# Performance work log

Hardware: AMD Instinct MI355X
Metric: run time of the kernel (lower is better)

The kernel has to match this reference:

```python
import jax, jax.numpy as jnp
import numpy as np


def setup_inputs() -> dict:
    key = jax.random.key(0)
    k1, k2, k3 = jax.random.split(key, 3)
    T, B, C, H, W = 8, 4, 128, 96, 96
    h = w = 384  # original visibility-map resolution
    values = jax.random.normal(k1, (T + 1, B, C, H, W), jnp.float32)
    tvmap = jax.random.uniform(k2, (B, 1, h, w), jnp.float32)
    rvmaps = jax.random.uniform(k3, (T, B, 1, h, w), jnp.float32)
    return {"values": values, "tvmap": tvmap, "rvmaps": rvmaps}


def _resize_bin(m, H, W):
    # bilinear resize (half-pixel centers == torch align_corners=False), then > 0.5 threshold
    r = jax.image.resize(m, m.shape[:-2] + (H, W), method="bilinear")
    return (r > 0.5).astype(m.dtype)


def reference(values, tvmap, rvmaps):
    t_feat = values[0]          # [B,C,H,W]
    r_feats = values[1:]        # [T,B,C,H,W]
    T, B, C, H, W = r_feats.shape

    tv = _resize_bin(tvmap, H, W)                           # [B,1,H,W]
    rv = jax.vmap(lambda m: _resize_bin(m, H, W))(rvmaps)   # [T,B,1,H,W]
    vmap_ = tv[None] * rv                                   # [T,B,1,H,W]

    # per-frame masked similarity score gs
    gs = jnp.sum(vmap_ * t_feat[None] * r_feats, axis=(-1, -2, -3))  # [T,B]
    v_sum = jnp.sum(vmap_[:, :, 0], axis=(-1, -2))                   # [T,B]
    empty = v_sum < 1e-4
    gs = jnp.where(empty, 0.0, gs) / (v_sum + empty.astype(gs.dtype)) / C

    gss = gs.transpose(1, 0)[:, None, :, None, None]   # [B,1,T,1,1]
    vmaps = rv.transpose(1, 2, 0, 3, 4)                # [B,1,T,H,W]

    # masked softmax over frame axis (dim=2) with zero-guard
    mv = gss * vmaps
    mx = jnp.max(mv, axis=2, keepdims=True)
    me = jnp.exp(mv - mx) * vmaps
    ms = jnp.sum(me, axis=2, keepdims=True)
    ms = ms + (ms < 1e-4).astype(ms.dtype)
    c_match = jax.lax.stop_gradient(me / ms)           # [B,1,T,H,W]

    rf = r_feats.transpose(1, 2, 0, 3, 4)              # [B,C,T,H,W]
    c_out = jnp.sum(rf * c_match, axis=2)              # [B,C,H,W]

    c_mask = jnp.sum(c_match * vmaps, axis=2)          # [B,1,H,W]
    c_mask = jax.lax.stop_gradient(1.0 - jnp.mean(c_mask, axis=1, keepdims=True))

    out = jnp.concatenate([t_feat, c_out, c_mask], axis=1)  # [B, 2C+1, H, W]
    return out, c_mask, gs
```

## Files before the change

kernel.cpp:

```cpp
#include <hip/hip_runtime.h>
#include <math.h>

#define T_ 8
#define B_ 4
#define C_ 128
#define HW_ 9216
#define IN_HW_ 147456

__device__ __forceinline__ double resize_px(const float* __restrict__ img, int y, int x) {
  static const double wm[8]  = {0.03125, 0.09375, 0.15625, 0.21875,
                                0.21875, 0.15625, 0.09375, 0.03125};
  static const double w0[8]  = {0.0, 0.0, 0.625/3.5, 0.875/3.5,
                                0.875/3.5, 0.625/3.5, 0.375/3.5, 0.125/3.5};
  static const double w95[8] = {0.125/3.5, 0.375/3.5, 0.625/3.5, 0.875/3.5,
                                0.875/3.5, 0.625/3.5, 0.0, 0.0};
  const double* wy = (y == 0) ? w0 : (y == 95 ? w95 : wm);
  const double* wx = (x == 0) ? w0 : (x == 95 ? w95 : wm);
  double acc = 0.0;
#pragma unroll
  for (int ky = 0; ky < 8; ++ky) {
    double wyv = wy[ky];
    if (wyv == 0.0) continue;
    int jy = 4 * y - 2 + ky;
    const float* row = img + jy * 384;
    double ra = 0.0;
#pragma unroll
    for (int kx = 0; kx < 8; ++kx) {
      double wxv = wx[kx];
      if (wxv == 0.0) continue;
      int jx = 4 * x - 2 + kx;
      ra += wxv * (double)row[jx];
    }
    acc += wyv * ra;
  }
  return acc;
}

__device__ __forceinline__ float block_reduce_sum_256(float v) {
  __shared__ float s[256];
  s[threadIdx.x] = v;
  __syncthreads();
  for (int k = 128; k > 0; k >>= 1) {
    if (threadIdx.x < (unsigned)k) s[threadIdx.x] += s[threadIdx.x + k];
    __syncthreads();
  }
  return s[0];
}

__global__ void k_init(float* __restrict__ v_sum) {
  if (threadIdx.x < T_ * B_) v_sum[threadIdx.x] = 0.f;
}

__global__ void k_tv(const float* __restrict__ tvmap, float* __restrict__ tv) {
  int b = blockIdx.y;
  int p = blockIdx.x * 256 + threadIdx.x;
  const float* img = tvmap + (size_t)b * IN_HW_;
  int y = p / 96, x = p % 96;
  tv[(size_t)b * HW_ + p] = (resize_px(img, y, x) > 0.5) ? 1.0f : 0.0f;
}

__global__ void k_rv(const float* __restrict__ rvmaps, const float* __restrict__ tv,
                     float* __restrict__ rv, float* __restrict__ vm,
                     float* __restrict__ v_sum) {
  int tb = blockIdx.y;
  int b = tb % B_;
  int p = blockIdx.x * 256 + threadIdx.x;
  const float* img = rvmaps + (size_t)tb * IN_HW_;
  int y = p / 96, x = p % 96;
  float rvv = (resize_px(img, y, x) > 0.5) ? 1.0f : 0.0f;
  float vmv = rvv * tv[(size_t)b * HW_ + p];
  rv[(size_t)tb * HW_ + p] = rvv;
  vm[(size_t)tb * HW_ + p] = vmv;
  float s = block_reduce_sum_256(vmv);
  if (threadIdx.x == 0) atomicAdd(&v_sum[tb], s);
}

__global__ __launch_bounds__(256) void k_gs(const float* __restrict__ values,
                                            const float* __restrict__ vm,
                                            float* __restrict__ gs_part) {
  int blk = blockIdx.x;
  int c  = blk % C_;
  int tb = blk / C_;
  int b  = tb % B_;
  const float4* rf  = (const float4*)(values + ((size_t)(B_ + tb) * C_ + c) * HW_);
  const float4* tf  = (const float4*)(values + ((size_t)b * C_ + c) * HW_);
  const float4* vmp = (const float4*)(vm + (size_t)tb * HW_);
  float acc = 0.f;
  for (int i = threadIdx.x; i < HW_ / 4; i += 256) {
    float4 m = vmp[i];
    float4 a = tf[i];
    float4 r = rf[i];
    acc += m.x * a.x * r.x + m.y * a.y * r.y + m.z * a.z * r.z + m.w * a.w * r.w;
  }
  float s = block_reduce_sum_256(acc);
  if (threadIdx.x == 0) gs_part[blk] = s;
}

__global__ void k_gsfin(const float* __restrict__ gs_part, const float* __restrict__ v_sum,
                        float* __restrict__ gs, float* __restrict__ out_gs) {
  int i = threadIdx.x;
  if (i < T_ * B_) {
    float s = 0.f;
    for (int c = 0; c < C_; ++c) s += gs_part[i * C_ + c];
    float vs = v_sum[i];
    bool empty = vs < 1e-4f;
    float g = (empty ? 0.f : s) / (vs + (empty ? 1.f : 0.f)) / (float)C_;
    gs[i] = g;
    out_gs[i] = g;
  }
}

__global__ __launch_bounds__(256) void k_epi(const float* __restrict__ values,
                                             const float* __restrict__ rv,
                                             const float* __restrict__ gs,
                                             float* __restrict__ out,
                                             float* __restrict__ out_cmask) {
  int ctile = blockIdx.x;
  int ptile = blockIdx.y;
  int b     = blockIdx.z;
  __shared__ float gsh[T_];
  if (threadIdx.x < T_) gsh[threadIdx.x] = gs[threadIdx.x * B_ + b];
  __syncthreads();

  int p0 = ptile * 1024 + threadIdx.x * 4;

  float4 rv4[T_];
#pragma unroll
  for (int t = 0; t < T_; ++t)
    rv4[t] = *(const float4*)(rv + ((size_t)(t * B_ + b)) * HW_ + p0);

  float cm[T_][4];
  float cmask[4];
#pragma unroll
  for (int j = 0; j < 4; ++j) {
    float mv[T_];
    float mx = -1e30f;
#pragma unroll
    for (int t = 0; t < T_; ++t) {
      float rvv = ((const float*)&rv4[t])[j];
      mv[t] = gsh[t] * rvv;
      mx = fmaxf(mx, mv[t]);
    }
    float e[T_];
    float ms = 0.f;
#pragma unroll
    for (int t = 0; t < T_; ++t) {
      float rvv = ((const float*)&rv4[t])[j];
      e[t] = expf(mv[t] - mx) * rvv;
      ms += e[t];
    }
    if (ms < 1e-4f) ms += 1.f;
    float inv = 1.f / ms;
    float cs = 0.f;
#pragma unroll
    for (int t = 0; t < T_; ++t) {
      cm[t][j] = e[t] * inv;
      cs += cm[t][j] * ((const float*)&rv4[t])[j];
    }
    cmask[j] = 1.f - cs;
  }

  size_t outb = (size_t)b * 257 * HW_;
#pragma unroll 1
  for (int cc = 0; cc < 8; ++cc) {
    int c = ctile * 8 + cc;
    float4 tf = *(const float4*)(values + ((size_t)b * C_ + c) * HW_ + p0);
    *(float4*)(out + outb + (size_t)c * HW_ + p0) = tf;
    float4 acc = {0.f, 0.f, 0.f, 0.f};
#pragma unroll
    for (int t = 0; t < T_; ++t) {
      const float4 r = *(const float4*)(values +
          ((size_t)((1 + t) * B_ + b) * C_ + c) * HW_ + p0);
      acc.x += cm[t][0] * r.x;
      acc.y += cm[t][1] * r.y;
      acc.z += cm[t][2] * r.z;
      acc.w += cm[t][3] * r.w;
    }
    *(float4*)(out + outb + (size_t)(C_ + c) * HW_ + p0) = acc;
  }
  if (ctile == 0) {
    float4 cmv = {cmask[0], cmask[1], cmask[2], cmask[3]};
    *(float4*)(out + outb + (size_t)256 * HW_ + p0) = cmv;
    *(float4*)(out_cmask + (size_t)b * HW_ + p0) = cmv;
  }
}

extern "C" void kernel_launch(void* const* d_in, const int* in_sizes, int n_in,
                              void* d_out, int out_size, void* d_ws, size_t ws_size,
                              hipStream_t stream) {
  const float* values = (const float*)d_in[0];
  const float* tvmap  = (const float*)d_in[1];
  const float* rvmaps = (const float*)d_in[2];
  float* out = (float*)d_out;

  float* ws      = (float*)d_ws;
  float* tv      = ws;
  float* rv      = tv + (size_t)B_ * HW_;
  float* vm      = rv + (size_t)T_ * B_ * HW_;
  float* gs_part = vm + (size_t)T_ * B_ * HW_;
  float* v_sum   = gs_part + T_ * B_ * C_;
  float* gsar    = v_sum + T_ * B_;

  float* out_cmask = out + (size_t)B_ * 257 * HW_;
  float* out_gs    = out_cmask + (size_t)B_ * HW_;

  hipLaunchKernelGGL(k_init,  dim3(1),                dim3(64),  0, stream, v_sum);
  hipLaunchKernelGGL(k_tv,    dim3(HW_ / 256, B_),    dim3(256), 0, stream, tvmap, tv);
  hipLaunchKernelGGL(k_rv,    dim3(HW_ / 256, T_ * B_), dim3(256), 0, stream, rvmaps, tv, rv, vm, v_sum);
  hipLaunchKernelGGL(k_gs,    dim3(T_ * B_ * C_),     dim3(256), 0, stream, values, vm, gs_part);
  hipLaunchKernelGGL(k_gsfin, dim3(1),                dim3(64),  0, stream, gs_part, v_sum, gsar, out_gs);
  hipLaunchKernelGGL(k_epi,   dim3(16, 9, B_),        dim3(256), 0, stream, values, rv, gsar, out, out_cmask);
}
```

Baseline: 347.2 us.

## Restructure pipeline: fuse tv resize, reuse t_feat across frames, precompute softmax weights

Removes the separate tv-resize kernel by recomputing the tv resize inside the rv kernel. The gs kernel is re-tiled so each block loads t_feat once and reuses it across all 8 frames, and the final reduction becomes a parallel 256-thread kernel. Softmax weights and c_mask move into a new k_cm kernel that writes the weights to workspace, aliased over the now-dead vm buffer. The epilogue then only reads those weights, uses smaller channel tiles for more blocks, and writes output with nontemporal stores. Block reductions switch to wavefront shuffles.

```diff
diff --git a/kernel.cpp b/kernel.cpp
--- a/kernel.cpp
+++ b/kernel.cpp
@@ -6,6 +6,8 @@
 #define C_ 128
 #define HW_ 9216
 #define IN_HW_ 147456
+
+typedef float nat_f4 __attribute__((ext_vector_type(4)));
 
 __device__ __forceinline__ double resize_px(const float* __restrict__ img, int y, int x) {
   static const double wm[8]  = {0.03125, 0.09375, 0.15625, 0.21875,
@@ -36,152 +38,175 @@
   return acc;
 }
 
-__device__ __forceinline__ float block_reduce_sum_256(float v) {
-  __shared__ float s[256];
-  s[threadIdx.x] = v;
-  __syncthreads();
-  for (int k = 128; k > 0; k >>= 1) {
-    if (threadIdx.x < (unsigned)k) s[threadIdx.x] += s[threadIdx.x + k];
-    __syncthreads();
-  }
-  return s[0];
+__device__ __forceinline__ float block_sum_256(float v) {
+  v += __shfl_xor(v, 1);
+  v += __shfl_xor(v, 2);
+  v += __shfl_xor(v, 4);
+  v += __shfl_xor(v, 8);
+  v += __shfl_xor(v, 16);
+  v += __shfl_xor(v, 32);
+  __shared__ float s[4];
+  int lane = threadIdx.x & 63, wv = threadIdx.x >> 6;
+  if (lane == 0) s[wv] = v;
+  __syncthreads();
+  return s[0] + s[1] + s[2] + s[3];
 }
 
 __global__ void k_init(float* __restrict__ v_sum) {
   if (threadIdx.x < T_ * B_) v_sum[threadIdx.x] = 0.f;
 }
 
-__global__ void k_tv(const float* __restrict__ tvmap, float* __restrict__ tv) {
-  int b = blockIdx.y;
-  int p = blockIdx.x * 256 + threadIdx.x;
-  const float* img = tvmap + (size_t)b * IN_HW_;
-  int y = p / 96, x = p % 96;
-  tv[(size_t)b * HW_ + p] = (resize_px(img, y, x) > 0.5) ? 1.0f : 0.0f;
-}
-
-__global__ void k_rv(const float* __restrict__ rvmaps, const float* __restrict__ tv,
-                     float* __restrict__ rv, float* __restrict__ vm,
-                     float* __restrict__ v_sum) {
+__global__ __launch_bounds__(256) void k_rv(const float* __restrict__ rvmaps,
+                                            const float* __restrict__ tvmap,
+                                            float* __restrict__ rv, float* __restrict__ vm,
+                                            float* __restrict__ v_sum) {
   int tb = blockIdx.y;
   int b = tb % B_;
   int p = blockIdx.x * 256 + threadIdx.x;
-  const float* img = rvmaps + (size_t)tb * IN_HW_;
   int y = p / 96, x = p % 96;
-  float rvv = (resize_px(img, y, x) > 0.5) ? 1.0f : 0.0f;
-  float vmv = rvv * tv[(size_t)b * HW_ + p];
+  float rvv = (resize_px(rvmaps + (size_t)tb * IN_HW_, y, x) > 0.5) ? 1.0f : 0.0f;
+  float tvv = (resize_px(tvmap  + (size_t)b  * IN_HW_, y, x) > 0.5) ? 1.0f : 0.0f;
+  float vmv = rvv * tvv;
   rv[(size_t)tb * HW_ + p] = rvv;
   vm[(size_t)tb * HW_ + p] = vmv;
-  float s = block_reduce_sum_256(vmv);
+  float s = block_sum_256(vmv);
   if (threadIdx.x == 0) atomicAdd(&v_sum[tb], s);
 }
 
 __global__ __launch_bounds__(256) void k_gs(const float* __restrict__ values,
                                             const float* __restrict__ vm,
                                             float* __restrict__ gs_part) {
-  int blk = blockIdx.x;
-  int c  = blk % C_;
-  int tb = blk / C_;
-  int b  = tb % B_;
-  const float4* rf  = (const float4*)(values + ((size_t)(B_ + tb) * C_ + c) * HW_);
-  const float4* tf  = (const float4*)(values + ((size_t)b * C_ + c) * HW_);
-  const float4* vmp = (const float4*)(vm + (size_t)tb * HW_);
-  float acc = 0.f;
-  for (int i = threadIdx.x; i < HW_ / 4; i += 256) {
-    float4 m = vmp[i];
-    float4 a = tf[i];
-    float4 r = rf[i];
-    acc += m.x * a.x * r.x + m.y * a.y * r.y + m.z * a.z * r.z + m.w * a.w * r.w;
-  }
-  float s = block_reduce_sum_256(acc);
-  if (threadIdx.x == 0) gs_part[blk] = s;
-}
-
-__global__ void k_gsfin(const float* __restrict__ gs_part, const float* __restrict__ v_sum,
-                        float* __restrict__ gs, float* __restrict__ out_gs) {
-  int i = threadIdx.x;
-  if (i < T_ * B_) {
-    float s = 0.f;
-    for (int c = 0; c < C_; ++c) s += gs_part[i * C_ + c];
+  int ptile = blockIdx.x;
+  int c     = blockIdx.y;
+  int b     = blockIdx.z;
+  int p0 = ptile * 1024 + threadIdx.x * 4;
+  const float4 a = *(const float4*)(values + ((size_t)b * C_ + c) * HW_ + p0);
+  float acc[T_];
+#pragma unroll
+  for (int t = 0; t < T_; ++t) {
+    const float4 m = *(const float4*)(vm + ((size_t)(t * B_ + b)) * HW_ + p0);
+    const float4 r = *(const float4*)(values + ((size_t)((1 + t) * B_ + b) * C_ + c) * HW_ + p0);
+    acc[t] = m.x * a.x * r.x + m.y * a.y * r.y + m.z * a.z * r.z + m.w * a.w * r.w;
+  }
+  __shared__ float sred[4][T_];
+  int lane = threadIdx.x & 63, wv = threadIdx.x >> 6;
+#pragma unroll
+  for (int t = 0; t < T_; ++t) {
+    float v = acc[t];
+    v += __shfl_xor(v, 1);
+    v += __shfl_xor(v, 2);
+    v += __shfl_xor(v, 4);
+    v += __shfl_xor(v, 8);
+    v += __shfl_xor(v, 16);
+    v += __shfl_xor(v, 32);
+    if (lane == 0) sred[wv][t] = v;
+  }
+  __syncthreads();
+  if (threadIdx.x < T_) {
+    int t = threadIdx.x;
+    float s = sred[0][t] + sred[1][t] + sred[2][t] + sred[3][t];
+    gs_part[((size_t)(t * B_ + b) * C_ + c) * 9 + ptile] = s;
+  }
+}
+
+__global__ __launch_bounds__(256) void k_gsfin(const float* __restrict__ gs_part,
+                                               const float* __restrict__ v_sum,
+                                               float* __restrict__ gs,
+                                               float* __restrict__ out_gs) {
+  __shared__ float sred[32][8];
+  int tb = threadIdx.x >> 3, j = threadIdx.x & 7;
+  const float4* p = (const float4*)(gs_part + (size_t)tb * (C_ * 9) + j * 144);
+  float s = 0.f;
+#pragma unroll
+  for (int i = 0; i < 36; ++i) {
+    float4 v = p[i];
+    s += v.x + v.y + v.z + v.w;
+  }
+  sred[tb][j] = s;
+  __syncthreads();
+  if (threadIdx.x < 32) {
+    int i = threadIdx.x;
+    float t = 0.f;
+#pragma unroll
+    for (int k = 0; k < 8; ++k) t += sred[i][k];
     float vs = v_sum[i];
     bool empty = vs < 1e-4f;
-    float g = (empty ? 0.f : s) / (vs + (empty ? 1.f : 0.f)) / (float)C_;
+    float g = (empty ? 0.f : t) / (vs + (empty ? 1.f : 0.f)) / (float)C_;
     gs[i] = g;
     out_gs[i] = g;
   }
 }
 
+__global__ __launch_bounds__(256) void k_cm(const float* __restrict__ rv,
+                                            const float* __restrict__ gs,
+                                            float* __restrict__ cm,
+                                            float* __restrict__ out,
+                                            float* __restrict__ out_cmask) {
+  int b = blockIdx.y;
+  int p = blockIdx.x * 256 + threadIdx.x;
+  __shared__ float gsh[T_];
+  if (threadIdx.x < T_) gsh[threadIdx.x] = gs[threadIdx.x * B_ + b];
+  __syncthreads();
+  float rvv[T_], mv[T_];
+  float mx = -1e30f;
+#pragma unroll
+  for (int t = 0; t < T_; ++t) {
+    rvv[t] = rv[((size_t)(t * B_ + b)) * HW_ + p];
+    mv[t] = gsh[t] * rvv[t];
+    mx = fmaxf(mx, mv[t]);
+  }
+  float e[T_], ms = 0.f;
+#pragma unroll
+  for (int t = 0; t < T_; ++t) {
+    e[t] = expf(mv[t] - mx) * rvv[t];
+    ms += e[t];
+  }
+  if (ms < 1e-4f) ms += 1.f;
+  float inv = 1.f / ms, cs = 0.f;
+#pragma unroll
+  for (int t = 0; t < T_; ++t) {
+    float w = e[t] * inv;
+    cm[((size_t)(t * B_ + b)) * HW_ + p] = w;
+    cs += w * rvv[t];
+  }
+  float cmv = 1.f - cs;
+  size_t outb = (size_t)b * 257 * HW_;
+  out[outb + (size_t)256 * HW_ + p] = cmv;
+  out_cmask[(size_t)b * HW_ + p] = cmv;
+}
+
 __global__ __launch_bounds__(256) void k_epi(const float* __restrict__ values,
-                                             const float* __restrict__ rv,
-                                             const float* __restrict__ gs,
-                                             float* __restrict__ out,
-                                             float* __restrict__ out_cmask) {
+                                             const float* __restrict__ cm,
+                                             float* __restrict__ out) {
   int ctile = blockIdx.x;
   int ptile = blockIdx.y;
   int b     = blockIdx.z;
-  __shared__ float gsh[T_];
-  if (threadIdx.x < T_) gsh[threadIdx.x] = gs[threadIdx.x * B_ + b];
-  __syncthreads();
-
   int p0 = ptile * 1024 + threadIdx.x * 4;
 
-  float4 rv4[T_];
+  float4 w[T_];
 #pragma unroll
   for (int t = 0; t < T_; ++t)
-    rv4[t] = *(const float4*)(rv + ((size_t)(t * B_ + b)) * HW_ + p0);
-
-  float cm[T_][4];
-  float cmask[4];
-#pragma unroll
-  for (int j = 0; j < 4; ++j) {
-    float mv[T_];
-    float mx = -1e30f;
-#pragma unroll
-    for (int t = 0; t < T_; ++t) {
-      float rvv = ((const float*)&rv4[t])[j];
-      mv[t] = gsh[t] * rvv;
-      mx = fmaxf(mx, mv[t]);
-    }
-    float e[T_];
-    float ms = 0.f;
-#pragma unroll
-    for (int t = 0; t < T_; ++t) {
-      float rvv = ((const float*)&rv4[t])[j];
-      e[t] = expf(mv[t] - mx) * rvv;
-      ms += e[t];
-    }
-    if (ms < 1e-4f) ms += 1.f;
-    float inv = 1.f / ms;
-    float cs = 0.f;
-#pragma unroll
-    for (int t = 0; t < T_; ++t) {
-      cm[t][j] = e[t] * inv;
-      cs += cm[t][j] * ((const float*)&rv4[t])[j];
-    }
-    cmask[j] = 1.f - cs;
-  }
+    w[t] = *(const float4*)(cm + ((size_t)(t * B_ + b)) * HW_ + p0);
 
   size_t outb = (size_t)b * 257 * HW_;
 #pragma unroll 1
-  for (int cc = 0; cc < 8; ++cc) {
-    int c = ctile * 8 + cc;
-    float4 tf = *(const float4*)(values + ((size_t)b * C_ + c) * HW_ + p0);
-    *(float4*)(out + outb + (size_t)c * HW_ + p0) = tf;
+  for (int cc = 0; cc < 4; ++cc) {
+    int c = ctile * 4 + cc;
+    const float4 tf = *(const float4*)(values + ((size_t)b * C_ + c) * HW_ + p0);
+    nat_f4 tfn = {tf.x, tf.y, tf.z, tf.w};
+    __builtin_nontemporal_store(tfn, (nat_f4*)(out + outb + (size_t)c * HW_ + p0));
     float4 acc = {0.f, 0.f, 0.f, 0.f};
 #pragma unroll
     for (int t = 0; t < T_; ++t) {
       const float4 r = *(const float4*)(values +
           ((size_t)((1 + t) * B_ + b) * C_ + c) * HW_ + p0);
-      acc.x += cm[t][0] * r.x;
-      acc.y += cm[t][1] * r.y;
-      acc.z += cm[t][2] * r.z;
-      acc.w += cm[t][3] * r.w;
+      acc.x += w[t].x * r.x;
+      acc.y += w[t].y * r.y;
+      acc.z += w[t].z * r.z;
+      acc.w += w[t].w * r.w;
     }
-    *(float4*)(out + outb + (size_t)(C_ + c) * HW_ + p0) = acc;
-  }
-  if (ctile == 0) {
-    float4 cmv = {cmask[0], cmask[1], cmask[2], cmask[3]};
-    *(float4*)(out + outb + (size_t)256 * HW_ + p0) = cmv;
-    *(float4*)(out_cmask + (size_t)b * HW_ + p0) = cmv;
+    nat_f4 accn = {acc.x, acc.y, acc.z, acc.w};
+    __builtin_nontemporal_store(accn, (nat_f4*)(out + outb + (size_t)(C_ + c) * HW_ + p0));
   }
 }
 
@@ -194,20 +219,20 @@
   float* out = (float*)d_out;
 
   float* ws      = (float*)d_ws;
-  float* tv      = ws;
-  float* rv      = tv + (size_t)B_ * HW_;
+  float* rv      = ws;
   float* vm      = rv + (size_t)T_ * B_ * HW_;
+  float* cmw     = vm;
   float* gs_part = vm + (size_t)T_ * B_ * HW_;
-  float* v_sum   = gs_part + T_ * B_ * C_;
+  float* v_sum   = gs_part + (size_t)T_ * B_ * C_ * 9;
   float* gsar    = v_sum + T_ * B_;
 
   float* out_cmask = out + (size_t)B_ * 257 * HW_;
   float* out_gs    = out_cmask + (size_t)B_ * HW_;
 
-  hipLaunchKernelGGL(k_init,  dim3(1),                dim3(64),  0, stream, v_sum);
-  hipLaunchKernelGGL(k_tv,    dim3(HW_ / 256, B_),    dim3(256), 0, stream, tvmap, tv);
-  hipLaunchKernelGGL(k_rv,    dim3(HW_ / 256, T_ * B_), dim3(256), 0, stream, rvmaps, tv, rv, vm, v_sum);
-  hipLaunchKernelGGL(k_gs,    dim3(T_ * B_ * C_),     dim3(256), 0, stream, values, vm, gs_part);
-  hipLaunchKernelGGL(k_gsfin, dim3(1),                dim3(64),  0, stream, gs_part, v_sum, gsar, out_gs);
-  hipLaunchKernelGGL(k_epi,   dim3(16, 9, B_),        dim3(256), 0, stream, values, rv, gsar, out, out_cmask);
-}
+  hipLaunchKernelGGL(k_init,  dim3(1),                 dim3(64),  0, stream, v_sum);
+  hipLaunchKernelGGL(k_rv,    dim3(HW_ / 256, T_ * B_), dim3(256), 0, stream, rvmaps, tvmap, rv, vm, v_sum);
+  hipLaunchKernelGGL(k_gs,    dim3(9, C_, B_),         dim3(256), 0, stream, values, vm, gs_part);
+  hipLaunchKernelGGL(k_gsfin, dim3(1),                 dim3(256), 0, stream, gs_part, v_sum, gsar, out_gs);
+  hipLaunchKernelGGL(k_cm,    dim3(HW_ / 256, B_),     dim3(256), 0, stream, rv, gsar, cmw, out, out_cmask);
+  hipLaunchKernelGGL(k_epi,   dim3(32, 9, B_),         dim3(256), 0, stream, values, cmw, out);
+}
```

Result: no change. 349.2 us (+0.6%).
